# Performance work log

Measured on AMD Instinct MI355X. Metric: run time of the kernel, lower is better.

Reference implementation:

```python
import jax, jax.numpy as jnp
import numpy as np

DIM = 512
INNER = 512  # heads*dim_head = 8*64
SCALE = 64 ** -0.5  # dim_head^{-0.5}, applied to BOTH q and k as in the source


def setup_inputs() -> dict:
    key = jax.random.key(0)
    k1, k2, k3, k4 = jax.random.split(key, 4)
    x = jax.random.normal(k1, (8, 2048, DIM), dtype=jnp.float32)
    Wqkv = jax.random.normal(k2, (DIM, 3 * INNER), dtype=jnp.float32) * (DIM ** -0.5)
    Wout = jax.random.normal(k3, (INNER, DIM), dtype=jnp.float32) * (INNER ** -0.5)
    bout = jax.random.normal(k4, (DIM,), dtype=jnp.float32) * 0.01
    return {"x": x, "Wqkv": Wqkv, "Wout": Wout, "bout": bout}


def reference(x, Wqkv, Wout, bout):
    # fused QKV projection (no bias)
    qkv = jnp.einsum("bnd,de->bne", x, Wqkv)
    q, k, v = jnp.split(qkv, 3, axis=-1)
    # note: source scales BOTH q and k by dim_head^{-0.5}
    scores = jnp.einsum("bnd,bmd->bnm", q * SCALE, k * SCALE)  # [B,N,N]
    attn = jax.nn.softmax(scores, axis=-1)
    out = jnp.einsum("bnm,bmd->bnd", attn, v)
    # residual add, then output projection (dropout=0.0 -> identity)
    return jnp.einsum("bnd,de->bne", out + x, Wout) + bout
```

## Files before the change

### kernel.cpp

```cpp
#include <hip/hip_runtime.h>
#include <hip/hip_bf16.h>


typedef __attribute__((ext_vector_type(8))) short bf16x8;
typedef __attribute__((ext_vector_type(4))) float f32x4;

__device__ __forceinline__ unsigned short f2bf(float f) {
  unsigned u = __builtin_bit_cast(unsigned, f);
  u += 0x7fffu + ((u >> 16) & 1u);
  return (unsigned short)(u >> 16);
}
__device__ __forceinline__ float bf2f(unsigned short h) {
  unsigned u = ((unsigned)h) << 16;
  return __builtin_bit_cast(float, u);
}

__device__ __forceinline__ void async16(const unsigned short* g, unsigned short* l) {
  __builtin_amdgcn_global_load_lds(
      (const __attribute__((address_space(1))) unsigned int*)g,
      (__attribute__((address_space(3))) unsigned int*)l, 16, 0, 0);
}

__global__ __launch_bounds__(256) void prep_x(const float* __restrict__ X,
                                              unsigned short* __restrict__ XB) {
  const size_t base = ((size_t)blockIdx.x * 256 + threadIdx.x) * 16;
  f32x4 a0 = *(const f32x4*)&X[base];
  f32x4 a1 = *(const f32x4*)&X[base + 4];
  f32x4 a2 = *(const f32x4*)&X[base + 8];
  f32x4 a3 = *(const f32x4*)&X[base + 12];
  bf16x8 o0, o1;
#pragma unroll
  for (int j = 0; j < 4; ++j) {
    o0[j] = (short)f2bf(a0[j]);
    o0[4 + j] = (short)f2bf(a1[j]);
    o1[j] = (short)f2bf(a2[j]);
    o1[4 + j] = (short)f2bf(a3[j]);
  }
  *(bf16x8*)&XB[base] = o0;
  *(bf16x8*)&XB[base + 8] = o1;
}

__global__ __launch_bounds__(256) void prep_w(const float* __restrict__ W,
                                              unsigned short* __restrict__ WT) {
  const int t = threadIdx.x;
  const int c0 = blockIdx.x * 128 + (t & 15) * 8;
  const int k0 = blockIdx.y * 128 + (t >> 4) * 8;
  float r[8][8];
#pragma unroll
  for (int j = 0; j < 8; ++j) {
    f32x4 lo = *(const f32x4*)&W[(size_t)(k0 + j) * 1536 + c0];
    f32x4 hi = *(const f32x4*)&W[(size_t)(k0 + j) * 1536 + c0 + 4];
#pragma unroll
    for (int q = 0; q < 4; ++q) {
      r[j][q] = lo[q];
      r[j][4 + q] = hi[q];
    }
  }
#pragma unroll
  for (int i = 0; i < 8; ++i) {
    const float scl = (c0 + i < 1024) ? 0.125f : 1.0f;
    bf16x8 o;
#pragma unroll
    for (int j = 0; j < 8; ++j) o[j] = (short)f2bf(r[j][i] * scl);
    *(bf16x8*)&WT[(size_t)(c0 + i) * 512 + k0] = o;
  }
}

__global__ __launch_bounds__(256) void transpose_wout(const float* __restrict__ W,
                                                      unsigned short* __restrict__ WT) {
  const int t = threadIdx.x;
  const int c0 = blockIdx.x * 128 + (t & 15) * 8;
  const int k0 = blockIdx.y * 128 + (t >> 4) * 8;
  float r[8][8];
#pragma unroll
  for (int j = 0; j < 8; ++j) {
    f32x4 lo = *(const f32x4*)&W[(size_t)(k0 + j) * 512 + c0];
    f32x4 hi = *(const f32x4*)&W[(size_t)(k0 + j) * 512 + c0 + 4];
#pragma unroll
    for (int q = 0; q < 4; ++q) {
      r[j][q] = lo[q];
      r[j][4 + q] = hi[q];
    }
  }
#pragma unroll
  for (int i = 0; i < 8; ++i) {
    bf16x8 o;
#pragma unroll
    for (int j = 0; j < 8; ++j) o[j] = (short)f2bf(r[j][i]);
    *(bf16x8*)&WT[(size_t)(c0 + i) * 512 + k0] = o;
  }
}

__global__ __launch_bounds__(256) void transpose_v(const unsigned short* __restrict__ QKV,
                                                   unsigned short* __restrict__ VT) {
  const int t = threadIdx.x;
  const int m0 = blockIdx.x * 128 + (t & 15) * 8;
  const int d0 = blockIdx.y * 128 + (t >> 4) * 8;
  bf16x8 r[8];
#pragma unroll
  for (int j = 0; j < 8; ++j)
    r[j] = *(const bf16x8*)&QKV[(size_t)(m0 + j) * 1536 + 1024 + d0];
#pragma unroll
  for (int i = 0; i < 8; ++i) {
    bf16x8 o;
#pragma unroll
    for (int j = 0; j < 8; ++j) o[j] = r[j][i];
    *(bf16x8*)&VT[(size_t)(d0 + i) * 16384 + m0] = o;
  }
}


#define GEMM97_VARS                                            \
  const int tid = threadIdx.x;                                 \
  const int wave = tid >> 6, lane = tid & 63;                  \
  const int wr = wave >> 1, wc = wave & 1;                     \
  const int lg = lane >> 4, ll = lane & 15;                    \
  const int kk = lg * 8;                                       \
  const int srow = wave * 32 + (lane >> 2);                    \
  const int scol = (lane & 3) * 8;

#define GEMM97_BODY(AG, ASTR, BG, BSTR, KDIM)                                            \
  __shared__ __align__(16) unsigned short Asm[4096];                                     \
  __shared__ __align__(16) unsigned short Bsm[4096];                                     \
  GEMM97_VARS                                                                            \
  f32x4 acc[4][4];                                                                       \
  _Pragma("unroll") for (int i = 0; i < 4; ++i) _Pragma("unroll") for (int j = 0; j < 4; \
                                                                       ++j) acc[i][j] =  \
      (f32x4){0.f, 0.f, 0.f, 0.f};                                                       \
  for (int kt = 0; kt < KDIM; kt += 32) {                                                \
    async16(&AG[(size_t)srow * ASTR + kt + scol], &Asm[wave * 1024]);                    \
    async16(&AG[(size_t)(srow + 16) * ASTR + kt + scol], &Asm[wave * 1024 + 512]);       \
    async16(&BG[(size_t)srow * BSTR + kt + scol], &Bsm[wave * 1024]);                    \
    async16(&BG[(size_t)(srow + 16) * BSTR + kt + scol], &Bsm[wave * 1024 + 512]);       \
    __syncthreads();                                                                     \
    bf16x8 af[4], bfr[4];                                                                \
    _Pragma("unroll") for (int ai = 0; ai < 4; ++ai) af[ai] =                            \
        *(const bf16x8*)&Asm[(wr * 64 + ai * 16 + ll) * 32 + kk];                        \
    _Pragma("unroll") for (int bj = 0; bj < 4; ++bj) bfr[bj] =                           \
        *(const bf16x8*)&Bsm[(wc * 64 + bj * 16 + ll) * 32 + kk];                        \
    _Pragma("unroll") for (int ai = 0; ai < 4; ++ai) _Pragma("unroll") for (int bj = 0;  \
                                                                            bj < 4;      \
                                                                            ++bj)        \
        acc[ai][bj] =                                                                    \
        __builtin_amdgcn_mfma_f32_16x16x32_bf16(af[ai], bfr[bj], acc[ai][bj], 0, 0, 0);  \
    __syncthreads();                                                                     \
  }

__global__ __launch_bounds__(256, 3) void gemm_qkv97(const unsigned short* __restrict__ XB,
                                                     const unsigned short* __restrict__ WT,
                                                     unsigned short* __restrict__ QKV) {
  const int bid = blockIdx.x;
  const int qt = bid / 12, nt = bid - qt * 12;
  const unsigned short* Ag = XB + (size_t)(qt * 128) * 512;
  const unsigned short* Bg = WT + (size_t)(nt * 128) * 512;
  GEMM97_BODY(Ag, 512, Bg, 512, 512)
#pragma unroll
  for (int ai = 0; ai < 4; ++ai)
#pragma unroll
    for (int bj = 0; bj < 4; ++bj) {
      const int col = nt * 128 + wc * 64 + bj * 16 + ll;
#pragma unroll
      for (int r = 0; r < 4; ++r) {
        const int row = qt * 128 + wr * 64 + ai * 16 + lg * 4 + r;
        QKV[(size_t)row * 1536 + col] = f2bf(acc[ai][bj][r]);
      }
    }
}

__global__ __launch_bounds__(512) void sgemm256(const unsigned short* __restrict__ QKV,
                                                unsigned short* __restrict__ S,
                                                float* __restrict__ part) {
  __shared__ __align__(16) unsigned short Asm[2][16384];
  __shared__ __align__(16) unsigned short Bsm[2][16384];
  const int tid = threadIdx.x;
  const int wave = tid >> 6, lane = tid & 63;
  const int wr = wave >> 2, wc = wave & 3;
  const int lg = lane >> 4, ll = lane & 15;
  const int bid = blockIdx.x;
  const int b = bid & 7;
  const int idx = bid >> 3;
  const int kvt = idx & 7, qt = idx >> 3;
  const unsigned short* Ag = QKV + ((size_t)b * 2048 + qt * 256) * 1536;
  const unsigned short* Bg = QKV + ((size_t)b * 2048 + kvt * 256) * 1536 + 512;
  const int sr = wave * 8 + (lane >> 3);
  const int sc = (((lane & 7) ^ ((lane >> 3) & 7))) * 8;

  f32x4 acc[8][4];
#pragma unroll
  for (int i = 0; i < 8; ++i)
#pragma unroll
    for (int j = 0; j < 4; ++j) acc[i][j] = (f32x4){0.f, 0.f, 0.f, 0.f};

#define SG_STAGE(BUF, KT)                                                              \
  _Pragma("unroll") for (int i = 0; i < 4; ++i) {                                      \
    async16(&Ag[(size_t)(i * 64 + sr) * 1536 + (KT) + sc], &Asm[BUF][(i * 64 + wave * 8) * 64]); \
    async16(&Bg[(size_t)(i * 64 + sr) * 1536 + (KT) + sc], &Bsm[BUF][(i * 64 + wave * 8) * 64]); \
  }

  SG_STAGE(0, 0)
  int cur = 0;
  __syncthreads();
  for (int kt = 0; kt < 512; kt += 64) {
    if (kt + 64 < 512) {
      if (cur) { SG_STAGE(0, kt + 64) } else { SG_STAGE(1, kt + 64) }
    }
#pragma unroll
    for (int half = 0; half < 2; ++half) {
      const int kb = (((half * 4 + lg) ^ (ll & 7))) * 8;
      bf16x8 af[8], bf4[4];
#pragma unroll
      for (int ai = 0; ai < 8; ++ai)
        af[ai] = *(const bf16x8*)&Asm[cur][(wr * 128 + ai * 16 + ll) * 64 + kb];
#pragma unroll
      for (int bj = 0; bj < 4; ++bj)
        bf4[bj] = *(const bf16x8*)&Bsm[cur][(wc * 64 + bj * 16 + ll) * 64 + kb];
#pragma unroll
      for (int ai = 0; ai < 8; ++ai)
#pragma unroll
        for (int bj = 0; bj < 4; ++bj)
          acc[ai][bj] = __builtin_amdgcn_mfma_f32_16x16x32_bf16(af[ai], bf4[bj], acc[ai][bj], 0, 0, 0);
    }
    __syncthreads();
    cur ^= 1;
  }
#undef SG_STAGE

#pragma unroll
  for (int ai = 0; ai < 8; ++ai)
#pragma unroll
    for (int bj = 0; bj < 4; ++bj)
#pragma unroll
      for (int r = 0; r < 4; ++r) acc[ai][bj][r] = __expf(acc[ai][bj][r]);

#pragma unroll
  for (int ai = 0; ai < 8; ++ai)
#pragma unroll
    for (int r = 0; r < 4; ++r) {
      float se = (acc[ai][0][r] + acc[ai][1][r]) + (acc[ai][2][r] + acc[ai][3][r]);
      se += __shfl_xor(se, 1);
      se += __shfl_xor(se, 2);
      se += __shfl_xor(se, 4);
      se += __shfl_xor(se, 8);
      if (ll == 0) {
        const size_t rowg = (size_t)b * 2048 + qt * 256 + wr * 128 + ai * 16 + lg * 4 + r;
        part[rowg * 32 + kvt * 4 + wc] = se;
      }
    }

  unsigned short* Sg = S + (size_t)b * 2048 * 2048;
#pragma unroll
  for (int ai = 0; ai < 8; ++ai)
#pragma unroll
    for (int bj = 0; bj < 4; ++bj) {
      const int col = kvt * 256 + wc * 64 + bj * 16 + ll;
#pragma unroll
      for (int r = 0; r < 4; ++r) {
        const int row = qt * 256 + wr * 128 + ai * 16 + lg * 4 + r;
        Sg[(size_t)row * 2048 + col] = f2bf(acc[ai][bj][r]);
      }
    }
}

__global__ __launch_bounds__(256) void combine_l(const float* __restrict__ part,
                                                 float* __restrict__ invl) {
  const int row = blockIdx.x * 256 + threadIdx.x;
  float l = 0.f;
#pragma unroll
  for (int t = 0; t < 8; ++t) {
    f32x4 v = *(const f32x4*)&part[(size_t)row * 32 + t * 4];
    l += (v[0] + v[1]) + (v[2] + v[3]);
  }
  invl[row] = 1.0f / l;
}

__global__ __launch_bounds__(256, 3) void pvgemm97(const unsigned short* __restrict__ S,
                                                   const unsigned short* __restrict__ VT,
                                                   const float* __restrict__ X,
                                                   const float* __restrict__ invl,
                                                   unsigned short* __restrict__ RES) {
  __shared__ __align__(16) unsigned short Asm[2][8192];
  __shared__ __align__(16) unsigned short Bsm[2][8192];
  const int tid = threadIdx.x;
  const int wave = tid >> 6, lane = tid & 63;
  const int wr = wave >> 1, wc = wave & 1;
  const int lg = lane >> 4, ll = lane & 15;
  const int bid = blockIdx.x;
  const int b = bid & 7;
  const int idx = bid >> 3;
  const int dt = idx & 3, qt = idx >> 2;
  const unsigned short* Ag = S + (size_t)b * 2048 * 2048 + (size_t)(qt * 128) * 2048;
  const unsigned short* Bg = VT + (size_t)(dt * 128) * 16384 + (size_t)b * 2048;
  const int sr = wave * 32 + (lane >> 3);
  const int sc = (((lane & 7) ^ ((lane >> 3) & 7))) * 8;

  f32x4 acc[4][4];
#pragma unroll
  for (int i = 0; i < 4; ++i)
#pragma unroll
    for (int j = 0; j < 4; ++j) acc[i][j] = (f32x4){0.f, 0.f, 0.f, 0.f};

#define PV_STAGE(BUF, KT)                                                                   \
  _Pragma("unroll") for (int i = 0; i < 4; ++i) {                                           \
    async16(&Ag[(size_t)(sr + i * 8) * 2048 + (KT) + sc], &Asm[BUF][(wave * 32 + i * 8) * 64]);  \
    async16(&Bg[(size_t)(sr + i * 8) * 16384 + (KT) + sc], &Bsm[BUF][(wave * 32 + i * 8) * 64]); \
  }

  PV_STAGE(0, 0)
  int cur = 0;
  __syncthreads();
  for (int kt = 0; kt < 2048; kt += 64) {
    if (kt + 64 < 2048) {
      if (cur) { PV_STAGE(0, kt + 64) } else { PV_STAGE(1, kt + 64) }
    }
#pragma unroll
    for (int half = 0; half < 2; ++half) {
      const int kb = (((half * 4 + lg) ^ (ll & 7))) * 8;
      bf16x8 af[4], bf4[4];
#pragma unroll
      for (int ai = 0; ai < 4; ++ai)
        af[ai] = *(const bf16x8*)&Asm[cur][(wr * 64 + ai * 16 + ll) * 64 + kb];
#pragma unroll
      for (int bj = 0; bj < 4; ++bj)
        bf4[bj] = *(const bf16x8*)&Bsm[cur][(wc * 64 + bj * 16 + ll) * 64 + kb];
#pragma unroll
      for (int ai = 0; ai < 4; ++ai)
#pragma unroll
        for (int bj = 0; bj < 4; ++bj)
          acc[ai][bj] = __builtin_amdgcn_mfma_f32_16x16x32_bf16(af[ai], bf4[bj], acc[ai][bj], 0, 0, 0);
    }
    __syncthreads();
    cur ^= 1;
  }
#undef PV_STAGE

  const int rowbase = b * 2048 + qt * 128 + wr * 64;
  float il[4][4];
#pragma unroll
  for (int ai = 0; ai < 4; ++ai)
#pragma unroll
    for (int r = 0; r < 4; ++r) il[ai][r] = invl[rowbase + ai * 16 + lg * 4 + r];
#pragma unroll
  for (int ai = 0; ai < 4; ++ai)
#pragma unroll
    for (int bj = 0; bj < 4; ++bj) {
      const int col = dt * 128 + wc * 64 + bj * 16 + ll;
#pragma unroll
      for (int r = 0; r < 4; ++r) {
        const size_t row = (size_t)rowbase + ai * 16 + lg * 4 + r;
        const float val = acc[ai][bj][r] * il[ai][r] + X[row * 512 + col];
        RES[row * 1536 + 1024 + col] = f2bf(val);
      }
    }
}

__global__ __launch_bounds__(256, 3) void gemm_out97(const unsigned short* __restrict__ A,
                                                     const unsigned short* __restrict__ WT,
                                                     const float* __restrict__ bias,
                                                     float* __restrict__ OUT) {
  const int bid = blockIdx.x;
  const int dt = bid & 3, qt = bid >> 2;
  const unsigned short* Ag = A + (size_t)(qt * 128) * 1536 + 1024;
  const unsigned short* Bg = WT + (size_t)(dt * 128) * 512;
  GEMM97_BODY(Ag, 1536, Bg, 512, 512)
#pragma unroll
  for (int ai = 0; ai < 4; ++ai)
#pragma unroll
    for (int bj = 0; bj < 4; ++bj) {
      const int col = dt * 128 + wc * 64 + bj * 16 + ll;
      const float bv = bias[col];
#pragma unroll
      for (int r = 0; r < 4; ++r) {
        const int row = qt * 128 + wr * 64 + ai * 16 + lg * 4 + r;
        OUT[(size_t)row * 512 + col] = acc[ai][bj][r] + bv;
      }
    }
}

extern "C" void kernel_launch(void* const* d_in, const int* in_sizes, int n_in,
                              void* d_out, int out_size, void* d_ws, size_t ws_size,
                              hipStream_t stream) {
  const float* x = (const float*)d_in[0];
  const float* Wqkv = (const float*)d_in[1];
  const float* Wout = (const float*)d_in[2];
  const float* bout = (const float*)d_in[3];
  float* out = (float*)d_out;

  unsigned short* qkvb = (unsigned short*)d_ws;
  unsigned short* VT = qkvb + (size_t)16384 * 1536;
  unsigned short* S = VT + (size_t)512 * 16384;
  unsigned short* xb = S;
  unsigned short* WT = S + (size_t)16384 * 512;
  unsigned short* WoutT = VT;
  float* part = out;
  float* invl = out + (size_t)16384 * 32;

  prep_x<<<2048, 256, 0, stream>>>(x, xb);
  prep_w<<<dim3(12, 4), 256, 0, stream>>>(Wqkv, WT);
  gemm_qkv97<<<1536, 256, 0, stream>>>(xb, WT, qkvb);
  transpose_v<<<dim3(128, 4), 256, 0, stream>>>(qkvb, VT);
  sgemm256<<<512, 512, 0, stream>>>(qkvb, S, part);
  combine_l<<<64, 256, 0, stream>>>(part, invl);
  pvgemm97<<<512, 256, 0, stream>>>(S, VT, x, invl, qkvb);
  transpose_wout<<<dim3(4, 4), 256, 0, stream>>>(Wout, WoutT);
  gemm_out97<<<512, 256, 0, stream>>>(qkvb, WoutT, bout, out);
}
```

Baseline: 177.9 us.

## Split score GEMM main loop into four interleaved load/MFMA phases with priority hints

After: 180.2 us. No clear change (+1.3%).

```diff
diff --git a/kernel.cpp b/kernel.cpp
--- a/kernel.cpp
+++ b/kernel.cpp
@@ -20,6 +20,8 @@
       (const __attribute__((address_space(1))) unsigned int*)g,
       (__attribute__((address_space(3))) unsigned int*)l, 16, 0, 0);
 }
+
+__device__ __forceinline__ void bar() { asm volatile("s_barrier" ::: "memory"); }
 
 __global__ __launch_bounds__(256) void prep_x(const float* __restrict__ X,
                                               unsigned short* __restrict__ XB) {
@@ -184,6 +186,8 @@
   const unsigned short* Bg = QKV + ((size_t)b * 2048 + kvt * 256) * 1536 + 512;
   const int sr = wave * 8 + (lane >> 3);
   const int sc = (((lane & 7) ^ ((lane >> 3) & 7))) * 8;
+  const int kb0 = ((lg) ^ (ll & 7)) * 8;
+  const int kb1 = ((4 + lg) ^ (ll & 7)) * 8;
 
   f32x4 acc[8][4];
 #pragma unroll
@@ -191,39 +195,96 @@
 #pragma unroll
     for (int j = 0; j < 4; ++j) acc[i][j] = (f32x4){0.f, 0.f, 0.f, 0.f};
 
-#define SG_STAGE(BUF, KT)                                                              \
-  _Pragma("unroll") for (int i = 0; i < 4; ++i) {                                      \
-    async16(&Ag[(size_t)(i * 64 + sr) * 1536 + (KT) + sc], &Asm[BUF][(i * 64 + wave * 8) * 64]); \
-    async16(&Bg[(size_t)(i * 64 + sr) * 1536 + (KT) + sc], &Bsm[BUF][(i * 64 + wave * 8) * 64]); \
-  }
-
-  SG_STAGE(0, 0)
+  int aoff[8], boff[4];
+#pragma unroll
+  for (int i = 0; i < 8; ++i) aoff[i] = (wr * 128 + i * 16 + ll) * 64;
+#pragma unroll
+  for (int j = 0; j < 4; ++j) boff[j] = (wc * 64 + j * 16 + ll) * 64;
+
+#define SGA(BUF, KT, I) async16(&Ag[(size_t)((I)*64 + sr) * 1536 + (KT) + sc], \
+                                &Asm[BUF][((I)*64 + wave * 8) * 64])
+#define SGB(BUF, KT, I) async16(&Bg[(size_t)((I)*64 + sr) * 1536 + (KT) + sc], \
+                                &Bsm[BUF][((I)*64 + wave * 8) * 64])
+
+#pragma unroll
+  for (int i = 0; i < 4; ++i) { SGA(0, 0, i); SGB(0, 0, i); }
+  asm volatile("s_waitcnt vmcnt(0)" ::: "memory");
+  __syncthreads();
+
   int cur = 0;
-  __syncthreads();
-  for (int kt = 0; kt < 512; kt += 64) {
-    if (kt + 64 < 512) {
-      if (cur) { SG_STAGE(0, kt + 64) } else { SG_STAGE(1, kt + 64) }
-    }
-#pragma unroll
-    for (int half = 0; half < 2; ++half) {
-      const int kb = (((half * 4 + lg) ^ (ll & 7))) * 8;
-      bf16x8 af[8], bf4[4];
-#pragma unroll
-      for (int ai = 0; ai < 8; ++ai)
-        af[ai] = *(const bf16x8*)&Asm[cur][(wr * 128 + ai * 16 + ll) * 64 + kb];
+  for (int t = 0; t < 8; ++t) {
+    const int ktn = t * 64 + 64;
+    const int nxt = cur ^ 1;
+    bf16x8 af[4], af2[4], bfr[4];
+#pragma unroll
+    for (int ai = 0; ai < 4; ++ai) af[ai] = *(const bf16x8*)&Asm[cur][aoff[ai] + kb0];
+#pragma unroll
+    for (int bj = 0; bj < 4; ++bj) bfr[bj] = *(const bf16x8*)&Bsm[cur][boff[bj] + kb0];
+    if (t < 7) {
+#pragma unroll
+      for (int i = 0; i < 4; ++i) SGA(nxt, ktn, i);
+    }
+    bar();
+    asm volatile("s_waitcnt lgkmcnt(0)" ::: "memory");
+    __builtin_amdgcn_sched_barrier(0);
+    __builtin_amdgcn_s_setprio(1);
+#pragma unroll
+    for (int ai = 0; ai < 4; ++ai)
 #pragma unroll
       for (int bj = 0; bj < 4; ++bj)
-        bf4[bj] = *(const bf16x8*)&Bsm[cur][(wc * 64 + bj * 16 + ll) * 64 + kb];
-#pragma unroll
-      for (int ai = 0; ai < 8; ++ai)
-#pragma unroll
-        for (int bj = 0; bj < 4; ++bj)
-          acc[ai][bj] = __builtin_amdgcn_mfma_f32_16x16x32_bf16(af[ai], bf4[bj], acc[ai][bj], 0, 0, 0);
-    }
-    __syncthreads();
-    cur ^= 1;
-  }
-#undef SG_STAGE
+        acc[ai][bj] = __builtin_amdgcn_mfma_f32_16x16x32_bf16(af[ai], bfr[bj], acc[ai][bj], 0, 0, 0);
+    __builtin_amdgcn_s_setprio(0);
+    bar();
+#pragma unroll
+    for (int ai = 0; ai < 4; ++ai) af2[ai] = *(const bf16x8*)&Asm[cur][aoff[4 + ai] + kb0];
+    if (t < 7) {
+#pragma unroll
+      for (int i = 0; i < 4; ++i) SGB(nxt, ktn, i);
+    }
+    bar();
+    asm volatile("s_waitcnt lgkmcnt(0)" ::: "memory");
+    __builtin_amdgcn_sched_barrier(0);
+    __builtin_amdgcn_s_setprio(1);
+#pragma unroll
+    for (int ai = 0; ai < 4; ++ai)
+#pragma unroll
+      for (int bj = 0; bj < 4; ++bj)
+        acc[4 + ai][bj] = __builtin_amdgcn_mfma_f32_16x16x32_bf16(af2[ai], bfr[bj], acc[4 + ai][bj], 0, 0, 0);
+    __builtin_amdgcn_s_setprio(0);
+    bar();
+#pragma unroll
+    for (int ai = 0; ai < 4; ++ai) af[ai] = *(const bf16x8*)&Asm[cur][aoff[ai] + kb1];
+#pragma unroll
+    for (int bj = 0; bj < 4; ++bj) bfr[bj] = *(const bf16x8*)&Bsm[cur][boff[bj] + kb1];
+    bar();
+    asm volatile("s_waitcnt lgkmcnt(0)" ::: "memory");
+    __builtin_amdgcn_sched_barrier(0);
+    __builtin_amdgcn_s_setprio(1);
+#pragma unroll
+    for (int ai = 0; ai < 4; ++ai)
+#pragma unroll
+      for (int bj = 0; bj < 4; ++bj)
+        acc[ai][bj] = __builtin_amdgcn_mfma_f32_16x16x32_bf16(af[ai], bfr[bj], acc[ai][bj], 0, 0, 0);
+    __builtin_amdgcn_s_setprio(0);
+    bar();
+#pragma unroll
+    for (int ai = 0; ai < 4; ++ai) af2[ai] = *(const bf16x8*)&Asm[cur][aoff[4 + ai] + kb1];
+    bar();
+    asm volatile("s_waitcnt lgkmcnt(0)" ::: "memory");
+    __builtin_amdgcn_sched_barrier(0);
+    __builtin_amdgcn_s_setprio(1);
+#pragma unroll
+    for (int ai = 0; ai < 4; ++ai)
+#pragma unroll
+      for (int bj = 0; bj < 4; ++bj)
+        acc[4 + ai][bj] = __builtin_amdgcn_mfma_f32_16x16x32_bf16(af2[ai], bfr[bj], acc[4 + ai][bj], 0, 0, 0);
+    __builtin_amdgcn_s_setprio(0);
+    asm volatile("s_waitcnt vmcnt(0)" ::: "memory");
+    bar();
+    cur = nxt;
+  }
+#undef SGA
+#undef SGB
 
 #pragma unroll
   for (int ai = 0; ai < 8; ++ai)
```

## Fuse x bf16 conversion and V transpose into QKV projection GEMM

Applied to the files above, without the earlier changes.

After: 179.7 us. Within noise of the previous version (+1.1%).

```diff
diff --git a/kernel.cpp b/kernel.cpp
--- a/kernel.cpp
+++ b/kernel.cpp
@@ -4,6 +4,7 @@
 
 typedef __attribute__((ext_vector_type(8))) short bf16x8;
 typedef __attribute__((ext_vector_type(4))) float f32x4;
+typedef __attribute__((ext_vector_type(4))) unsigned short u16x4;
 
 __device__ __forceinline__ unsigned short f2bf(float f) {
   unsigned u = __builtin_bit_cast(unsigned, f);
@@ -19,25 +20,6 @@
   __builtin_amdgcn_global_load_lds(
       (const __attribute__((address_space(1))) unsigned int*)g,
       (__attribute__((address_space(3))) unsigned int*)l, 16, 0, 0);
-}
-
-__global__ __launch_bounds__(256) void prep_x(const float* __restrict__ X,
-                                              unsigned short* __restrict__ XB) {
-  const size_t base = ((size_t)blockIdx.x * 256 + threadIdx.x) * 16;
-  f32x4 a0 = *(const f32x4*)&X[base];
-  f32x4 a1 = *(const f32x4*)&X[base + 4];
-  f32x4 a2 = *(const f32x4*)&X[base + 8];
-  f32x4 a3 = *(const f32x4*)&X[base + 12];
-  bf16x8 o0, o1;
-#pragma unroll
-  for (int j = 0; j < 4; ++j) {
-    o0[j] = (short)f2bf(a0[j]);
-    o0[4 + j] = (short)f2bf(a1[j]);
-    o1[j] = (short)f2bf(a2[j]);
-    o1[4 + j] = (short)f2bf(a3[j]);
-  }
-  *(bf16x8*)&XB[base] = o0;
-  *(bf16x8*)&XB[base + 8] = o1;
 }
 
 __global__ __launch_bounds__(256) void prep_w(const float* __restrict__ W,
@@ -90,25 +72,6 @@
     *(bf16x8*)&WT[(size_t)(c0 + i) * 512 + k0] = o;
   }
 }
-
-__global__ __launch_bounds__(256) void transpose_v(const unsigned short* __restrict__ QKV,
-                                                   unsigned short* __restrict__ VT) {
-  const int t = threadIdx.x;
-  const int m0 = blockIdx.x * 128 + (t & 15) * 8;
-  const int d0 = blockIdx.y * 128 + (t >> 4) * 8;
-  bf16x8 r[8];
-#pragma unroll
-  for (int j = 0; j < 8; ++j)
-    r[j] = *(const bf16x8*)&QKV[(size_t)(m0 + j) * 1536 + 1024 + d0];
-#pragma unroll
-  for (int i = 0; i < 8; ++i) {
-    bf16x8 o;
-#pragma unroll
-    for (int j = 0; j < 8; ++j) o[j] = r[j][i];
-    *(bf16x8*)&VT[(size_t)(d0 + i) * 16384 + m0] = o;
-  }
-}
-
 
 #define GEMM97_VARS                                            \
   const int tid = threadIdx.x;                                 \
@@ -119,52 +82,87 @@
   const int srow = wave * 32 + (lane >> 2);                    \
   const int scol = (lane & 3) * 8;
 
-#define GEMM97_BODY(AG, ASTR, BG, BSTR, KDIM)                                            \
-  __shared__ __align__(16) unsigned short Asm[4096];                                     \
-  __shared__ __align__(16) unsigned short Bsm[4096];                                     \
-  GEMM97_VARS                                                                            \
-  f32x4 acc[4][4];                                                                       \
-  _Pragma("unroll") for (int i = 0; i < 4; ++i) _Pragma("unroll") for (int j = 0; j < 4; \
-                                                                       ++j) acc[i][j] =  \
-      (f32x4){0.f, 0.f, 0.f, 0.f};                                                       \
-  for (int kt = 0; kt < KDIM; kt += 32) {                                                \
-    async16(&AG[(size_t)srow * ASTR + kt + scol], &Asm[wave * 1024]);                    \
-    async16(&AG[(size_t)(srow + 16) * ASTR + kt + scol], &Asm[wave * 1024 + 512]);       \
-    async16(&BG[(size_t)srow * BSTR + kt + scol], &Bsm[wave * 1024]);                    \
-    async16(&BG[(size_t)(srow + 16) * BSTR + kt + scol], &Bsm[wave * 1024 + 512]);       \
-    __syncthreads();                                                                     \
-    bf16x8 af[4], bfr[4];                                                                \
-    _Pragma("unroll") for (int ai = 0; ai < 4; ++ai) af[ai] =                            \
-        *(const bf16x8*)&Asm[(wr * 64 + ai * 16 + ll) * 32 + kk];                        \
-    _Pragma("unroll") for (int bj = 0; bj < 4; ++bj) bfr[bj] =                           \
-        *(const bf16x8*)&Bsm[(wc * 64 + bj * 16 + ll) * 32 + kk];                        \
-    _Pragma("unroll") for (int ai = 0; ai < 4; ++ai) _Pragma("unroll") for (int bj = 0;  \
-                                                                            bj < 4;      \
-                                                                            ++bj)        \
-        acc[ai][bj] =                                                                    \
-        __builtin_amdgcn_mfma_f32_16x16x32_bf16(af[ai], bfr[bj], acc[ai][bj], 0, 0, 0);  \
-    __syncthreads();                                                                     \
-  }
-
-__global__ __launch_bounds__(256, 3) void gemm_qkv97(const unsigned short* __restrict__ XB,
-                                                     const unsigned short* __restrict__ WT,
-                                                     unsigned short* __restrict__ QKV) {
+__global__ __launch_bounds__(256, 3) void gemm_qkv_fused(const float* __restrict__ X,
+                                                         const unsigned short* __restrict__ WT,
+                                                         unsigned short* __restrict__ QKV,
+                                                         unsigned short* __restrict__ VT) {
+  __shared__ __align__(16) unsigned short Asm[4096];
+  __shared__ __align__(16) unsigned short Bsm[4096];
+  GEMM97_VARS
   const int bid = blockIdx.x;
   const int qt = bid / 12, nt = bid - qt * 12;
-  const unsigned short* Ag = XB + (size_t)(qt * 128) * 512;
+  const float* Ag = X + (size_t)(qt * 128) * 512;
   const unsigned short* Bg = WT + (size_t)(nt * 128) * 512;
-  GEMM97_BODY(Ag, 512, Bg, 512, 512)
-#pragma unroll
-  for (int ai = 0; ai < 4; ++ai)
-#pragma unroll
-    for (int bj = 0; bj < 4; ++bj) {
-      const int col = nt * 128 + wc * 64 + bj * 16 + ll;
-#pragma unroll
-      for (int r = 0; r < 4; ++r) {
-        const int row = qt * 128 + wr * 64 + ai * 16 + lg * 4 + r;
-        QKV[(size_t)row * 1536 + col] = f2bf(acc[ai][bj][r]);
-      }
-    }
+
+  f32x4 acc[4][4];
+#pragma unroll
+  for (int i = 0; i < 4; ++i)
+#pragma unroll
+    for (int j = 0; j < 4; ++j) acc[i][j] = (f32x4){0.f, 0.f, 0.f, 0.f};
+
+  f32x4 ar0 = *(const f32x4*)&Ag[(size_t)srow * 512 + scol];
+  f32x4 ar1 = *(const f32x4*)&Ag[(size_t)srow * 512 + scol + 4];
+  f32x4 ar2 = *(const f32x4*)&Ag[(size_t)(srow + 16) * 512 + scol];
+  f32x4 ar3 = *(const f32x4*)&Ag[(size_t)(srow + 16) * 512 + scol + 4];
+
+  for (int kt = 0; kt < 512; kt += 32) {
+    async16(&Bg[(size_t)srow * 512 + kt + scol], &Bsm[wave * 1024]);
+    async16(&Bg[(size_t)(srow + 16) * 512 + kt + scol], &Bsm[wave * 1024 + 512]);
+    bf16x8 a0, a1;
+#pragma unroll
+    for (int j = 0; j < 4; ++j) {
+      a0[j] = (short)f2bf(ar0[j]);
+      a0[4 + j] = (short)f2bf(ar1[j]);
+      a1[j] = (short)f2bf(ar2[j]);
+      a1[4 + j] = (short)f2bf(ar3[j]);
+    }
+    *(bf16x8*)&Asm[srow * 32 + scol] = a0;
+    *(bf16x8*)&Asm[(srow + 16) * 32 + scol] = a1;
+    __syncthreads();
+    if (kt + 32 < 512) {
+      ar0 = *(const f32x4*)&Ag[(size_t)srow * 512 + kt + 32 + scol];
+      ar1 = *(const f32x4*)&Ag[(size_t)srow * 512 + kt + 32 + scol + 4];
+      ar2 = *(const f32x4*)&Ag[(size_t)(srow + 16) * 512 + kt + 32 + scol];
+      ar3 = *(const f32x4*)&Ag[(size_t)(srow + 16) * 512 + kt + 32 + scol + 4];
+    }
+    bf16x8 af[4], bfr[4];
+#pragma unroll
+    for (int ai = 0; ai < 4; ++ai) af[ai] = *(const bf16x8*)&Asm[(wr * 64 + ai * 16 + ll) * 32 + kk];
+#pragma unroll
+    for (int bj = 0; bj < 4; ++bj) bfr[bj] = *(const bf16x8*)&Bsm[(wc * 64 + bj * 16 + ll) * 32 + kk];
+#pragma unroll
+    for (int ai = 0; ai < 4; ++ai)
+#pragma unroll
+      for (int bj = 0; bj < 4; ++bj)
+        acc[ai][bj] = __builtin_amdgcn_mfma_f32_16x16x32_bf16(af[ai], bfr[bj], acc[ai][bj], 0, 0, 0);
+    __syncthreads();
+  }
+
+  if (nt < 8) {
+#pragma unroll
+    for (int ai = 0; ai < 4; ++ai)
+#pragma unroll
+      for (int bj = 0; bj < 4; ++bj) {
+        const int col = nt * 128 + wc * 64 + bj * 16 + ll;
+#pragma unroll
+        for (int r = 0; r < 4; ++r) {
+          const int row = qt * 128 + wr * 64 + ai * 16 + lg * 4 + r;
+          QKV[(size_t)row * 1536 + col] = f2bf(acc[ai][bj][r]);
+        }
+      }
+  } else {
+#pragma unroll
+    for (int ai = 0; ai < 4; ++ai)
+#pragma unroll
+      for (int bj = 0; bj < 4; ++bj) {
+        const int d = (nt - 8) * 128 + wc * 64 + bj * 16 + ll;
+        const int row0 = qt * 128 + wr * 64 + ai * 16 + lg * 4;
+        u16x4 o;
+#pragma unroll
+        for (int r = 0; r < 4; ++r) o[r] = f2bf(acc[ai][bj][r]);
+        *(u16x4*)&VT[(size_t)d * 16384 + row0] = o;
+      }
+  }
 }
 
 __global__ __launch_bounds__(512) void sgemm256(const unsigned short* __restrict__ QKV,
@@ -357,11 +355,36 @@
                                                      const unsigned short* __restrict__ WT,
                                                      const float* __restrict__ bias,
                                                      float* __restrict__ OUT) {
+  __shared__ __align__(16) unsigned short Asm[4096];
+  __shared__ __align__(16) unsigned short Bsm[4096];
+  GEMM97_VARS
   const int bid = blockIdx.x;
   const int dt = bid & 3, qt = bid >> 2;
   const unsigned short* Ag = A + (size_t)(qt * 128) * 1536 + 1024;
   const unsigned short* Bg = WT + (size_t)(dt * 128) * 512;
-  GEMM97_BODY(Ag, 1536, Bg, 512, 512)
+  f32x4 acc[4][4];
+#pragma unroll
+  for (int i = 0; i < 4; ++i)
+#pragma unroll
+    for (int j = 0; j < 4; ++j) acc[i][j] = (f32x4){0.f, 0.f, 0.f, 0.f};
+  for (int kt = 0; kt < 512; kt += 32) {
+    async16(&Ag[(size_t)srow * 1536 + kt + scol], &Asm[wave * 1024]);
+    async16(&Ag[(size_t)(srow + 16) * 1536 + kt + scol], &Asm[wave * 1024 + 512]);
+    async16(&Bg[(size_t)srow * 512 + kt + scol], &Bsm[wave * 1024]);
+    async16(&Bg[(size_t)(srow + 16) * 512 + kt + scol], &Bsm[wave * 1024 + 512]);
+    __syncthreads();
+    bf16x8 af[4], bfr[4];
+#pragma unroll
+    for (int ai = 0; ai < 4; ++ai) af[ai] = *(const bf16x8*)&Asm[(wr * 64 + ai * 16 + ll) * 32 + kk];
+#pragma unroll
+    for (int bj = 0; bj < 4; ++bj) bfr[bj] = *(const bf16x8*)&Bsm[(wc * 64 + bj * 16 + ll) * 32 + kk];
+#pragma unroll
+    for (int ai = 0; ai < 4; ++ai)
+#pragma unroll
+      for (int bj = 0; bj < 4; ++bj)
+        acc[ai][bj] = __builtin_amdgcn_mfma_f32_16x16x32_bf16(af[ai], bfr[bj], acc[ai][bj], 0, 0, 0);
+    __syncthreads();
+  }
 #pragma unroll
   for (int ai = 0; ai < 4; ++ai)
 #pragma unroll
@@ -388,19 +411,16 @@
   unsigned short* qkvb = (unsigned short*)d_ws;
   unsigned short* VT = qkvb + (size_t)16384 * 1536;
   unsigned short* S = VT + (size_t)512 * 16384;
-  unsigned short* xb = S;
-  unsigned short* WT = S + (size_t)16384 * 512;
-  unsigned short* WoutT = VT;
+  unsigned short* WT = S;
+  unsigned short* WoutT = S + (size_t)1536 * 512;
   float* part = out;
   float* invl = out + (size_t)16384 * 32;
 
-  prep_x<<<2048, 256, 0, stream>>>(x, xb);
   prep_w<<<dim3(12, 4), 256, 0, stream>>>(Wqkv, WT);
-  gemm_qkv97<<<1536, 256, 0, stream>>>(xb, WT, qkvb);
-  transpose_v<<<dim3(128, 4), 256, 0, stream>>>(qkvb, VT);
+  gemm_qkv_fused<<<1536, 256, 0, stream>>>(x, WT, qkvb, VT);
   sgemm256<<<512, 512, 0, stream>>>(qkvb, S, part);
   combine_l<<<64, 256, 0, stream>>>(part, invl);
   pvgemm97<<<512, 256, 0, stream>>>(S, VT, x, invl, qkvb);
-  transpose_wout<<<dim3(4, 4), 256, 0, stream>>>(Wout, WoutT);
-  gemm_out97<<<512, 256, 0, stream>>>(qkvb, WoutT, bout, out);
-}
+  transpose_wout<<<dim3(4, 4), 256, 0, stream>>>(Wout, (unsigned short*)S);
+  gemm_out97<<<512, 256, 0, stream>>>(qkvb, (unsigned short*)S, bout, out);
+}
```
